# Kernel tuning notes

Hardware: AMD Instinct MI355X
Metric: run time of the kernel (lower is better)

Reference implementation:

```python
import jax, jax.numpy as jnp
import numpy as np

K_TOP = 4
NUM_EXPERTS = 8


def _lstm_dir(x, wih, whh, b):
    # x: [B,T,in], wih: [4H,in], whh: [4H,H], b: [4H] (b_ih+b_hh)
    xW = jnp.einsum('bti,gi->btg', x, wih) + b  # [B,T,4H]
    B = x.shape[0]
    H = whh.shape[1]
    init = (jnp.zeros((B, H), x.dtype), jnp.zeros((B, H), x.dtype))

    def step(carry, xt):
        h, c = carry
        g = xt + h @ whh.T
        i, f, gg, o = jnp.split(g, 4, axis=-1)  # torch gate order i,f,g,o
        c = jax.nn.sigmoid(f) * c + jax.nn.sigmoid(i) * jnp.tanh(gg)
        h = jax.nn.sigmoid(o) * jnp.tanh(c)
        return (h, c), h

    _, hs = jax.lax.scan(step, init, jnp.swapaxes(xW, 0, 1))  # [T,B,H]
    return jnp.swapaxes(hs, 0, 1)


def _bidir_layer(x, Wih, Whh, bih, bhh):
    # Wih: [2,4H,in]; dir 0 forward, dir 1 backward
    hf = _lstm_dir(x, Wih[0], Whh[0], bih[0] + bhh[0])
    hb = _lstm_dir(x[:, ::-1], Wih[1], Whh[1], bih[1] + bhh[1])[:, ::-1]
    return jnp.concatenate([hf, hb], axis=-1)  # [B,T,2H]


def _expert(x, Wih0, Whh0, bih0, bhh0, Wih1, Whh1, bih1, bhh1):
    h = _bidir_layer(x, Wih0, Whh0, bih0, bhh0)   # [B,T,2H]
    h = _bidir_layer(h, Wih1, Whh1, bih1, bhh1)   # [B,T,2H]
    return h


def _cv_squared(v):
    v = v.astype(jnp.float32)
    return jnp.var(v, ddof=1) / (jnp.mean(v) ** 2 + 1e-10)


def _forward(x, spk, wg_w, wg_b, Wih0, Whh0, bih0, bhh0, Wih1, Whh1, bih1, bhh1, fc1_w, fc1_b, fc_w, fc_b, loss_coef=0.01):
    B, T, _ = x.shape
    # --- top-k gating (eval path: clean logits, no noise) ---
    logits = spk @ wg_w.T + wg_b                      # [B,E]
    top_vals, top_idx = jax.lax.top_k(logits, K_TOP + 1)
    gates_k = jax.nn.softmax(top_vals[:, :K_TOP], axis=-1)
    rows = jnp.arange(B)[:, None]
    gates = jnp.zeros_like(logits).at[rows, top_idx[:, :K_TOP]].set(gates_k)  # [B,E]
    load = (gates > 0).sum(0)
    importance = gates.sum(0)
    loss = (_cv_squared(importance) + _cv_squared(load)) * loss_coef
    # --- run all experts (dense mixture, as in source) ---
    expert_h = jax.vmap(_expert, in_axes=(None, 0, 0, 0, 0, 0, 0, 0, 0))(
        x, Wih0, Whh0, bih0, bhh0, Wih1, Whh1, bih1, bhh1)          # [E,B,T,2H]
    expert_out = jnp.einsum('ebtf,hf->ebth', expert_h, fc1_w) + fc1_b  # [E,B,T,H]
    data_output = jnp.einsum('ebth,be->bth', expert_out, gates)        # [B,T,H]
    out = jnp.einsum('bth,oh->bto', data_output, fc_w) + fc_b          # [B,T,O]
    out = jnp.swapaxes(out, 0, 1)                                      # [T,B,O]
    return out, loss


def setup_inputs() -> dict:
    key = jax.random.key(0)
    ks = jax.random.split(key, 16)
    B, T, D, H, E, O, S = 32, 1024, 128, 128, 8, 44, 256
    s = 0.08  # weight scale to keep LSTM gates in sane range
    return {
        'x': jax.random.normal(ks[0], (B, T, D), jnp.float32),
        'spk': jax.random.normal(ks[1], (B, S), jnp.float32),
        'wg_w': jax.random.normal(ks[2], (E, S), jnp.float32) * s,
        'wg_b': jax.random.normal(ks[3], (E,), jnp.float32) * s,
        'Wih0': jax.random.normal(ks[4], (E, 2, 4 * H, D), jnp.float32) * s,
        'Whh0': jax.random.normal(ks[5], (E, 2, 4 * H, H), jnp.float32) * s,
        'bih0': jax.random.normal(ks[6], (E, 2, 4 * H), jnp.float32) * s,
        'bhh0': jax.random.normal(ks[7], (E, 2, 4 * H), jnp.float32) * s,
        'Wih1': jax.random.normal(ks[8], (E, 2, 4 * H, 2 * H), jnp.float32) * s,
        'Whh1': jax.random.normal(ks[9], (E, 2, 4 * H, H), jnp.float32) * s,
        'bih1': jax.random.normal(ks[10], (E, 2, 4 * H), jnp.float32) * s,
        'bhh1': jax.random.normal(ks[11], (E, 2, 4 * H), jnp.float32) * s,
        'fc1_w': jax.random.normal(ks[12], (H, 2 * H), jnp.float32) * s,
        'fc1_b': jax.random.normal(ks[13], (H,), jnp.float32) * s,
        'fc_w': jax.random.normal(ks[14], (O, H), jnp.float32) * s,
        'fc_b': jax.random.normal(ks[15], (O,), jnp.float32) * s,
    }


def reference(x, spk, wg_w, wg_b, Wih0, Whh0, bih0, bhh0, Wih1, Whh1, bih1, bhh1, fc1_w, fc1_b, fc_w, fc_b):
    return _forward(x, spk, wg_w, wg_b, Wih0, Whh0, bih0, bhh0, Wih1, Whh1, bih1, bhh1, fc1_w, fc1_b, fc_w, fc_b)
```

## Files before the change

### kernel.cpp

```cpp
#include <hip/hip_runtime.h>

typedef __attribute__((ext_vector_type(4))) float f32x4;
typedef __attribute__((ext_vector_type(8))) short s16x8;

#define LOG2E 1.4426950408889634f

__device__ __forceinline__ unsigned short f2bf(float f) {
  union { float f; unsigned int i; } v; v.f = f;
  unsigned int u = v.i;
  u = (u + 0x7FFFu + ((u >> 16) & 1u)) >> 16;
  return (unsigned short)u;
}
__device__ __forceinline__ float bf2f(unsigned short s) {
  union { unsigned int i; float f; } v; v.i = ((unsigned int)s) << 16;
  return v.f;
}
__device__ __forceinline__ float rcp_(float x) { return __builtin_amdgcn_rcpf(x); }
__device__ __forceinline__ float ex2(float x) { return __builtin_amdgcn_exp2f(x); }
__device__ __forceinline__ f32x4 mfma16(s16x8 a, s16x8 b, f32x4 c) {
  return __builtin_amdgcn_mfma_f32_16x16x32_bf16(a, b, c, 0, 0, 0);
}
__device__ __forceinline__ s16x8 pack8(const float* s) {
  s16x8 v;
#pragma unroll
  for (int j = 0; j < 8; ++j) v[j] = (short)f2bf(s[j]);
  return v;
}

#define OFF_H0  0
#define OFF_XW  134217728
#define OFF_XT  201326592
#define OFF_WHH 209715200
#define OFF_HST 213909504
#define OFF_CST 214040576
#define OFF_M   214564864
#define OFF_CV  214614016
#define OFF_G   214614272
#define WS_NEED 214615296

__global__ void wsdbg_kernel(float* __restrict__ out, float v) { out[0] = v; }

__global__ void prepw_kernel(const float* __restrict__ Whh0, const float* __restrict__ Whh1,
                             unsigned short* __restrict__ whhb) {
  const int i = blockIdx.x * 512 + threadIdx.x;
  if (i < 2097152)
    whhb[i] = f2bf(i < 1048576 ? Whh0[i] : Whh1[i - 1048576]);
}

__global__ void prepx_kernel(const float* __restrict__ x, unsigned short* __restrict__ xt) {
  const int i = blockIdx.x * 512 + threadIdx.x;
  for (int j = i; j < 4194304; j += 2097152) {
    const int b = j >> 17, rem = j & 131071, t = rem >> 7, f = rem & 127;
    xt[((size_t)t * 32 + b) * 128 + f] = f2bf(x[j]);
  }
}

__global__ void mprep_kernel(const float* __restrict__ fc1w, const float* __restrict__ fc1b,
                             const float* __restrict__ fcw, const float* __restrict__ fcb,
                             float* __restrict__ M, float* __restrict__ Cv) {
  const int mi = blockIdx.x * 256 + threadIdx.x;
  if (mi < 12288) {
    const int dd = mi / 6144, rem = mi % 6144, o = rem >> 7, hc = rem & 127;
    float s = 0.f;
    if (o < 44)
      for (int h = 0; h < 128; ++h) s += fcw[o * 128 + h] * fc1w[h * 256 + dd * 128 + hc];
    M[mi] = s;
  }
  if (blockIdx.x == 0 && threadIdx.x < 44) {
    const int o = threadIdx.x;
    float s = fcb[o];
    for (int h = 0; h < 128; ++h) s += fcw[o * 128 + h] * fc1b[h];
    Cv[o] = s;
  }
}

__global__ void initout_kernel(const float* __restrict__ Cv, float* __restrict__ out) {
  const int i = blockIdx.x * 512 + threadIdx.x;
  if (i < 1441792) out[i] = Cv[i % 44];
}

__global__ void gating_kernel(const float* __restrict__ spk,
                              const float* __restrict__ wgw,
                              const float* __restrict__ wgb,
                              float* __restrict__ gates_out,
                              float* __restrict__ loss_out) {
  __shared__ __align__(16) float logits[32][8];
  __shared__ __align__(16) float gmat[32][8];
  const int tid = threadIdx.x;
  {
    const int b = tid >> 3, e = tid & 7;
    float s = wgb[e];
    for (int k = 0; k < 256; ++k) s += spk[b * 256 + k] * wgw[e * 256 + k];
    logits[b][e] = s;
  }
  __syncthreads();
  if (tid < 32) {
    const int b = tid;
    float v[8];
    for (int e = 0; e < 8; ++e) v[e] = logits[b][e];
    int idx[4]; float val[4];
    unsigned used = 0;
    for (int k = 0; k < 4; ++k) {
      float best = -1e30f; int bi = 0;
      for (int e = 0; e < 8; ++e)
        if (!((used >> e) & 1) && v[e] > best) { best = v[e]; bi = e; }
      used |= (1u << bi); idx[k] = bi; val[k] = best;
    }
    const float m = val[0];
    float ex[4], ssum = 0.f;
    for (int k = 0; k < 4; ++k) { ex[k] = ex2(LOG2E * (val[k] - m)); ssum += ex[k]; }
    for (int e = 0; e < 8; ++e) gmat[b][e] = 0.f;
    for (int k = 0; k < 4; ++k) gmat[b][idx[k]] = ex[k] / ssum;
    for (int e = 0; e < 8; ++e) gates_out[b * 8 + e] = gmat[b][e];
  }
  __syncthreads();
  if (tid == 0) {
    float imp[8], ld[8];
    for (int e = 0; e < 8; ++e) {
      float si = 0.f, sl = 0.f;
      for (int b = 0; b < 32; ++b) { si += gmat[b][e]; sl += (gmat[b][e] > 0.f) ? 1.f : 0.f; }
      imp[e] = si; ld[e] = sl;
    }
    float mi = 0.f, ml = 0.f;
    for (int e = 0; e < 8; ++e) { mi += imp[e]; ml += ld[e]; }
    mi *= 0.125f; ml *= 0.125f;
    float vi = 0.f, vl = 0.f;
    for (int e = 0; e < 8; ++e) {
      vi += (imp[e] - mi) * (imp[e] - mi);
      vl += (ld[e] - ml) * (ld[e] - ml);
    }
    vi /= 7.f; vl /= 7.f;
    loss_out[0] = 0.01f * (vi / (mi * mi + 1e-10f) + vl / (ml * ml + 1e-10f));
  }
}

template <int L>
__global__ __launch_bounds__(512, 1) void fused(
    int k,
    const unsigned short* __restrict__ Asrc,
    const float* __restrict__ Wih, const float* __restrict__ bihp, const float* __restrict__ bhhp,
    const unsigned short* __restrict__ whhb,
    unsigned short* __restrict__ xwbufs,
    unsigned short* __restrict__ hstate, float* __restrict__ cstate,
    unsigned short* __restrict__ h0out,
    const float* __restrict__ Mmat, const float* __restrict__ gatesp,
    float* __restrict__ outp) {
  constexpr int KC = L ? 8 : 4;
  constexpr int KS = KC * 32;
  const int tid = threadIdx.x, w = tid >> 6, l = tid & 63;
  const int l15 = l & 15, lq = l >> 4;

  if (blockIdx.x >= 32) {
    if (k >= 16) return;
    const int gb = blockIdx.x - 32;
    const int ed = gb & 15, e = ed >> 1, d = ed & 1;
    const int slice = gb >> 4;
    unsigned short* xw = xwbufs + (size_t)(k & 1) * 16777216;

    s16x8 bf[4][KC];
    float bias[4];
#pragma unroll
    for (int j = 0; j < 4; ++j) {
      const int n = w * 64 + j * 16 + l15;
      bias[j] = bihp[ed * 512 + n] + bhhp[ed * 512 + n];
      const float* wp = Wih + ((size_t)ed * 512 + n) * KS + lq * 8;
#pragma unroll
      for (int kc = 0; kc < KC; ++kc) bf[j][kc] = pack8(wp + kc * 32);
    }
    for (int ss = slice; ss < 64; ss += 14) {
      const int s = k * 64 + ss;
      const int t = d ? 1023 - s : s;
#pragma unroll
      for (int mt = 0; mt < 2; ++mt) {
        const size_t arow = (size_t)(L ? (e * 1024 + t) : t) * 32 + mt * 16 + l15;
        const unsigned short* ap = Asrc + arow * KS + lq * 8;
        s16x8 af[KC];
#pragma unroll
        for (int kc = 0; kc < KC; ++kc) af[kc] = *(const s16x8*)(ap + kc * 32);
        f32x4 acc[4];
#pragma unroll
        for (int j = 0; j < 4; ++j) acc[j] = f32x4{bias[j], bias[j], bias[j], bias[j]};
#pragma unroll
        for (int kc = 0; kc < KC; ++kc) {
#pragma unroll
          for (int j = 0; j < 4; ++j) acc[j] = mfma16(af[kc], bf[j][kc], acc[j]);
        }
        unsigned short* op = xw + (((size_t)(ed * 2 + mt) * 64 + ss) * 512) * 16 + lq * 4;
#pragma unroll
        for (int j = 0; j < 4; ++j) {
          const int n = w * 64 + j * 16 + l15;
          ushort4 o4;
          o4.x = f2bf(acc[j][0]); o4.y = f2bf(acc[j][1]);
          o4.z = f2bf(acc[j][2]); o4.w = f2bf(acc[j][3]);
          *(ushort4*)(op + (size_t)n * 16) = o4;
        }
      }
    }
    return;
  }

  if (k == 0) return;
  const int c = k - 1;
  const int rb = blockIdx.x, ed2 = rb >> 1, bh = rb & 1;
  const int e = ed2 >> 1, d = ed2 & 1;
  __shared__ __align__(16) char hbf[2][4096];
  const int cell = w * 16 + l15;

  s16x8 bfh[4][4];
#pragma unroll
  for (int g = 0; g < 4; ++g) {
    const unsigned short* wp = whhb + ((size_t)ed2 * 512 + g * 128 + cell) * 128 + lq * 8;
#pragma unroll
    for (int kc = 0; kc < 4; ++kc) bfh[g][kc] = *(const s16x8*)(wp + kc * 32);
  }
  s16x8 mfr[4];
  float g4[4] = {0.f, 0.f, 0.f, 0.f};
  if constexpr (L) {
    if (w < 3) {
      const float* mp = Mmat + ((size_t)d * 48 + w * 16 + l15) * 128 + lq * 8;
#pragma unroll
      for (int kc = 0; kc < 4; ++kc) mfr[kc] = pack8(mp + kc * 32);
    }
#pragma unroll
    for (int r = 0; r < 4; ++r) g4[r] = gatesp[(bh * 16 + lq * 4 + r) * 8 + e];
  }

  const int wbase = ((cell >> 5) << 10) | (((cell >> 3) & 3) << 8) | ((cell & 7) << 1);
  float cst[4];
  if (c == 0) {
#pragma unroll
    for (int r = 0; r < 4; ++r) cst[r] = 0.f;
    if (tid < 256) {
      s16x8 z = {0, 0, 0, 0, 0, 0, 0, 0};
      *(s16x8*)(&hbf[0][tid * 16]) = z;
    }
  } else {
    const float* cp = cstate + ((size_t)rb * 512 + tid) * 4;
    const unsigned short* hp = hstate + ((size_t)rb * 512 + tid) * 4;
#pragma unroll
    for (int r = 0; r < 4; ++r) {
      cst[r] = cp[r];
      *(unsigned short*)(&hbf[0][wbase + (lq * 4 + r) * 16]) = hp[r];
    }
  }
  __syncthreads();

  const unsigned short* xwr = xwbufs + (size_t)(c & 1) * 16777216;
  const unsigned short* xwb = xwr + ((size_t)(ed2 * 2 + bh) * 64) * 8192 + cell * 16 + lq * 4;
  const size_t hob = (size_t)e * 8388608 + (size_t)(bh * 16 + lq * 4) * 256 + (size_t)d * 128 + cell;

  ushort4 xqA[4], xqB[4];
#pragma unroll
  for (int g = 0; g < 4; ++g) {
    xqA[g] = *(const ushort4*)(xwb + g * 2048);
    xqB[g] = *(const ushort4*)(xwb + 8192 + g * 2048);
  }

  auto step = [&](int tt, ushort4* xq, int tpre) {
    const int p = tt & 1;
    s16x8 hf[4];
#pragma unroll
    for (int kc = 0; kc < 4; ++kc) hf[kc] = *(const s16x8*)(&hbf[p][kc * 1024 + l * 16]);
    f32x4 a[4];
#pragma unroll
    for (int g = 0; g < 4; ++g) {
      a[g][0] = bf2f(xq[g].x); a[g][1] = bf2f(xq[g].y);
      a[g][2] = bf2f(xq[g].z); a[g][3] = bf2f(xq[g].w);
    }
    if (tpre < 64) {
#pragma unroll
      for (int g = 0; g < 4; ++g) xq[g] = *(const ushort4*)(xwb + (size_t)tpre * 8192 + g * 2048);
    }
    f32x4 mo = {0.f, 0.f, 0.f, 0.f};
    if constexpr (L) {
      if (w < 3) {
#pragma unroll
        for (int kc = 0; kc < 4; ++kc) mo = mfma16(hf[kc], mfr[kc], mo);
      }
    }
#pragma unroll
    for (int kc = 0; kc < 4; ++kc) {
#pragma unroll
      for (int g = 0; g < 4; ++g) a[g] = mfma16(hf[kc], bfh[g][kc], a[g]);
    }
    const int s = c * 64 + tt;
    unsigned short hb4[4];
#pragma unroll
    for (int r = 0; r < 4; ++r) {
      const float gi = a[0][r], gf = a[1][r], gg = a[2][r], go = a[3][r];
      const float ai = ex2(-LOG2E * gi);
      const float af2 = ex2(-LOG2E * gf);
      const float ao = ex2(-LOG2E * go);
      const float bg = ex2(fminf(2.f * LOG2E * gg, 126.f));
      const float sf = rcp_(1.f + af2);
      const float itg = (bg - 1.f) * rcp_((1.f + ai) * (1.f + bg));
      const float cc = sf * cst[r] + itg;
      cst[r] = cc;
      const float qc = ex2(fminf(2.f * LOG2E * cc, 126.f));
      const float hv = (qc - 1.f) * rcp_((1.f + ao) * (1.f + qc));
      hb4[r] = f2bf(hv);
    }
    char* hw = &hbf[1 - p][0];
#pragma unroll
    for (int r = 0; r < 4; ++r) *(unsigned short*)(hw + wbase + (lq * 4 + r) * 16) = hb4[r];
    if constexpr (!L) {
      const int t = d ? 1023 - s : s;
      unsigned short* hp = h0out + hob + (size_t)t * 8192;
#pragma unroll
      for (int r = 0; r < 4; ++r) hp[r * 256] = hb4[r];
    } else {
      if (w < 3 && s > 0) {
        const int o = w * 16 + l15;
        if (o < 44) {
          const int tp = d ? (1024 - s) : (s - 1);
#pragma unroll
          for (int r = 0; r < 4; ++r)
            atomicAdd(&outp[((size_t)tp * 32 + bh * 16 + lq * 4 + r) * 44 + o], g4[r] * mo[r]);
        }
      }
    }
    if (tt == 63) {
      unsigned short* hsp = hstate + ((size_t)rb * 512 + tid) * 4;
      float* csp = cstate + ((size_t)rb * 512 + tid) * 4;
#pragma unroll
      for (int r = 0; r < 4; ++r) { hsp[r] = hb4[r]; csp[r] = cst[r]; }
    }
    __syncthreads();
  };

  for (int t2 = 0; t2 < 64; t2 += 2) {
    step(t2, xqA, t2 + 2);
    step(t2 + 1, xqB, t2 + 3);
  }

  if constexpr (L) {
    if (k == 16 && w < 3) {
      s16x8 hf[4];
#pragma unroll
      for (int kc = 0; kc < 4; ++kc) hf[kc] = *(const s16x8*)(&hbf[0][kc * 1024 + l * 16]);
      f32x4 mo = {0.f, 0.f, 0.f, 0.f};
#pragma unroll
      for (int kc = 0; kc < 4; ++kc) mo = mfma16(hf[kc], mfr[kc], mo);
      const int o = w * 16 + l15;
      if (o < 44) {
        const int tp = d ? 0 : 1023;
#pragma unroll
        for (int r = 0; r < 4; ++r)
          atomicAdd(&outp[((size_t)tp * 32 + bh * 16 + lq * 4 + r) * 44 + o], g4[r] * mo[r]);
      }
    }
  }
}

extern "C" void kernel_launch(void* const* d_in, const int* in_sizes, int n_in,
                              void* d_out, int out_size, void* d_ws, size_t ws_size,
                              hipStream_t stream) {
  const float* x    = (const float*)d_in[0];
  const float* spk  = (const float*)d_in[1];
  const float* wgw  = (const float*)d_in[2];
  const float* wgb  = (const float*)d_in[3];
  const float* Wih0 = (const float*)d_in[4];
  const float* Whh0 = (const float*)d_in[5];
  const float* bih0 = (const float*)d_in[6];
  const float* bhh0 = (const float*)d_in[7];
  const float* Wih1 = (const float*)d_in[8];
  const float* Whh1 = (const float*)d_in[9];
  const float* bih1 = (const float*)d_in[10];
  const float* bhh1 = (const float*)d_in[11];
  const float* fc1w = (const float*)d_in[12];
  const float* fc1b = (const float*)d_in[13];
  const float* fcw  = (const float*)d_in[14];
  const float* fcb  = (const float*)d_in[15];
  float* out = (float*)d_out;

  if (ws_size < (size_t)WS_NEED) {
    wsdbg_kernel<<<1, 1, 0, stream>>>(out, (float)(ws_size >> 20));
    return;
  }
  char* ws = (char*)d_ws;
  unsigned short* h0     = (unsigned short*)(ws + OFF_H0);
  unsigned short* xwbufs = (unsigned short*)(ws + OFF_XW);
  unsigned short* xt     = (unsigned short*)(ws + OFF_XT);
  unsigned short* whhb   = (unsigned short*)(ws + OFF_WHH);
  unsigned short* hstate = (unsigned short*)(ws + OFF_HST);
  float*          cstate = (float*)(ws + OFF_CST);
  float*          Mmat   = (float*)(ws + OFF_M);
  float*          Cv     = (float*)(ws + OFF_CV);
  float*          gatesw = (float*)(ws + OFF_G);

  prepw_kernel<<<4096, 512, 0, stream>>>(Whh0, Whh1, whhb);
  prepx_kernel<<<4096, 512, 0, stream>>>(x, xt);
  mprep_kernel<<<48, 256, 0, stream>>>(fc1w, fc1b, fcw, fcb, Mmat, Cv);
  initout_kernel<<<2816, 512, 0, stream>>>(Cv, out);
  gating_kernel<<<1, 256, 0, stream>>>(spk, wgw, wgb, gatesw, out + 1441792);

  for (int k = 0; k <= 16; ++k)
    fused<0><<<256, 512, 0, stream>>>(k, xt, Wih0, bih0, bhh0, whhb, xwbufs,
                                      hstate, cstate, h0, nullptr, nullptr, out);
  for (int k = 0; k <= 16; ++k)
    fused<1><<<256, 512, 0, stream>>>(k, h0, Wih1, bih1, bhh1, whhb + 1048576, xwbufs,
                                      hstate, cstate, nullptr, Mmat, gatesw, out);
}
```

Measured before the change: 2.409 ms.

## Move layer-1 output projection to dedicated blocks and prescale gate weights

Gate weights and biases are now pre-multiplied by the exp2 scale factors, so the recurrent step's activation math needs fewer multiplies. The per-step output projection and atomicAdd in layer 1 are moved out of the recurrent blocks into separate blocks (192+). Those blocks process a double-buffered chunk of saved hidden states one launch later, reduce over experts with gate weights, and write output with plain adds. The recurrent step is rewritten as a single loop with the hidden-state store deferred by one step, and an extra launch is added to drain the pipeline. This trades more workspace and reduced input-projection parallelism in layer 1 for a shorter serial critical path.

```diff
diff --git a/kernel.cpp b/kernel.cpp
--- a/kernel.cpp
+++ b/kernel.cpp
@@ -4,6 +4,7 @@
 typedef __attribute__((ext_vector_type(8))) short s16x8;
 
 #define LOG2E 1.4426950408889634f
+#define K2L   2.8853900817779268f
 
 __device__ __forceinline__ unsigned short f2bf(float f) {
   union { float f; unsigned int i; } v; v.f = f;
@@ -20,31 +21,35 @@
 __device__ __forceinline__ f32x4 mfma16(s16x8 a, s16x8 b, f32x4 c) {
   return __builtin_amdgcn_mfma_f32_16x16x32_bf16(a, b, c, 0, 0, 0);
 }
-__device__ __forceinline__ s16x8 pack8(const float* s) {
+__device__ __forceinline__ s16x8 pack8s(const float* s, float sc) {
   s16x8 v;
 #pragma unroll
-  for (int j = 0; j < 8; ++j) v[j] = (short)f2bf(s[j]);
+  for (int j = 0; j < 8; ++j) v[j] = (short)f2bf(s[j] * sc);
   return v;
 }
 
-#define OFF_H0  0
-#define OFF_XW  134217728
-#define OFF_XT  201326592
-#define OFF_WHH 209715200
-#define OFF_HST 213909504
-#define OFF_CST 214040576
-#define OFF_M   214564864
-#define OFF_CV  214614016
-#define OFF_G   214614272
-#define WS_NEED 214615296
+#define OFF_H0   0
+#define OFF_XW   134217728
+#define OFF_XT   201326592
+#define OFF_WHH  209715200
+#define OFF_H1C  213909504
+#define OFF_HST  230686720
+#define OFF_CST  230817792
+#define OFF_M    231079936
+#define OFF_CV   231129088
+#define OFF_G    231129344
+#define WS_NEED  231130368
 
 __global__ void wsdbg_kernel(float* __restrict__ out, float v) { out[0] = v; }
 
 __global__ void prepw_kernel(const float* __restrict__ Whh0, const float* __restrict__ Whh1,
                              unsigned short* __restrict__ whhb) {
   const int i = blockIdx.x * 512 + threadIdx.x;
-  if (i < 2097152)
-    whhb[i] = f2bf(i < 1048576 ? Whh0[i] : Whh1[i - 1048576]);
+  if (i < 2097152) {
+    const int gate = (i >> 14) & 3;
+    const float sc = (gate == 2) ? K2L : -LOG2E;
+    whhb[i] = f2bf((i < 1048576 ? Whh0[i] : Whh1[i - 1048576]) * sc);
+  }
 }
 
 __global__ void prepx_kernel(const float* __restrict__ x, unsigned short* __restrict__ xt) {
@@ -142,7 +147,7 @@
     const unsigned short* __restrict__ whhb,
     unsigned short* __restrict__ xwbufs,
     unsigned short* __restrict__ hstate, float* __restrict__ cstate,
-    unsigned short* __restrict__ h0out,
+    unsigned short* __restrict__ hout,
     const float* __restrict__ Mmat, const float* __restrict__ gatesp,
     float* __restrict__ outp) {
   constexpr int KC = L ? 8 : 4;
@@ -150,11 +155,59 @@
   const int tid = threadIdx.x, w = tid >> 6, l = tid & 63;
   const int l15 = l & 15, lq = l >> 4;
 
+  if (L && blockIdx.x >= 192) {
+    const int c2 = k - 2;
+    if (c2 < 0 || c2 > 15) return;
+    if (w >= 6) return;
+    const int ss = blockIdx.x - 192;
+    const int mt = (w >= 3) ? 1 : 0, ot = w - mt * 3;
+    const int o = ot * 16 + l15;
+    const bool ov = o < 44;
+    s16x8 bfm[2][4];
+#pragma unroll
+    for (int dd = 0; dd < 2; ++dd)
+#pragma unroll
+      for (int kc = 0; kc < 4; ++kc) {
+        if (ov) bfm[dd][kc] = pack8s(Mmat + ((size_t)dd * 48 + o) * 128 + kc * 32 + lq * 8, 1.f);
+        else { s16x8 z = {0,0,0,0,0,0,0,0}; bfm[dd][kc] = z; }
+      }
+    const unsigned short* hb = hout + (size_t)(c2 & 1) * 4194304;
+    f32x4 acc0 = {0.f,0.f,0.f,0.f}, acc1 = {0.f,0.f,0.f,0.f};
+    for (int e = 0; e < 8; ++e) {
+      const unsigned short* ap = hb + ((((size_t)e * 64 + ss) * 32) + mt * 16 + l15) * 256 + lq * 8;
+      f32x4 p0 = {0.f,0.f,0.f,0.f}, p1 = {0.f,0.f,0.f,0.f};
+#pragma unroll
+      for (int kc = 0; kc < 4; ++kc) {
+        s16x8 a0 = *(const s16x8*)(ap + kc * 32);
+        s16x8 a1 = *(const s16x8*)(ap + 128 + kc * 32);
+        p0 = mfma16(a0, bfm[0][kc], p0);
+        p1 = mfma16(a1, bfm[1][kc], p1);
+      }
+#pragma unroll
+      for (int r = 0; r < 4; ++r) {
+        const float g = gatesp[(mt * 16 + lq * 4 + r) * 8 + e];
+        acc0[r] += g * p0[r];
+        acc1[r] += g * p1[r];
+      }
+    }
+    if (ov) {
+      const int s2 = c2 * 64 + ss, t1 = 1023 - s2;
+#pragma unroll
+      for (int r = 0; r < 4; ++r) {
+        const int b = mt * 16 + lq * 4 + r;
+        outp[((size_t)s2 * 32 + b) * 44 + o] += acc0[r];
+        outp[((size_t)t1 * 32 + b) * 44 + o] += acc1[r];
+      }
+    }
+    return;
+  }
+
   if (blockIdx.x >= 32) {
     if (k >= 16) return;
     const int gb = blockIdx.x - 32;
     const int ed = gb & 15, e = ed >> 1, d = ed & 1;
     const int slice = gb >> 4;
+    const int nsl = L ? 10 : 14;
     unsigned short* xw = xwbufs + (size_t)(k & 1) * 16777216;
 
     s16x8 bf[4][KC];
@@ -162,12 +215,13 @@
 #pragma unroll
     for (int j = 0; j < 4; ++j) {
       const int n = w * 64 + j * 16 + l15;
-      bias[j] = bihp[ed * 512 + n] + bhhp[ed * 512 + n];
+      const float sc = ((n >> 7) == 2) ? K2L : -LOG2E;
+      bias[j] = (bihp[ed * 512 + n] + bhhp[ed * 512 + n]) * sc;
       const float* wp = Wih + ((size_t)ed * 512 + n) * KS + lq * 8;
 #pragma unroll
-      for (int kc = 0; kc < KC; ++kc) bf[j][kc] = pack8(wp + kc * 32);
-    }
-    for (int ss = slice; ss < 64; ss += 14) {
+      for (int kc = 0; kc < KC; ++kc) bf[j][kc] = pack8s(wp + kc * 32, sc);
+    }
+    for (int ss = slice; ss < 64; ss += nsl) {
       const int s = k * 64 + ss;
       const int t = d ? 1023 - s : s;
 #pragma unroll
@@ -199,8 +253,8 @@
     return;
   }
 
-  if (k == 0) return;
   const int c = k - 1;
+  if (c < 0 || c > 15) return;
   const int rb = blockIdx.x, ed2 = rb >> 1, bh = rb & 1;
   const int e = ed2 >> 1, d = ed2 & 1;
   __shared__ __align__(16) char hbf[2][4096];
@@ -213,25 +267,14 @@
 #pragma unroll
     for (int kc = 0; kc < 4; ++kc) bfh[g][kc] = *(const s16x8*)(wp + kc * 32);
   }
-  s16x8 mfr[4];
-  float g4[4] = {0.f, 0.f, 0.f, 0.f};
-  if constexpr (L) {
-    if (w < 3) {
-      const float* mp = Mmat + ((size_t)d * 48 + w * 16 + l15) * 128 + lq * 8;
-#pragma unroll
-      for (int kc = 0; kc < 4; ++kc) mfr[kc] = pack8(mp + kc * 32);
-    }
-#pragma unroll
-    for (int r = 0; r < 4; ++r) g4[r] = gatesp[(bh * 16 + lq * 4 + r) * 8 + e];
-  }
-
-  const int wbase = ((cell >> 5) << 10) | (((cell >> 3) & 3) << 8) | ((cell & 7) << 1);
+  const int wb0 = ((cell >> 5) << 10) | (((cell >> 3) & 3) << 8) | ((cell & 7) << 1);
   float cst[4];
+  unsigned short hb4[4];
   if (c == 0) {
 #pragma unroll
-    for (int r = 0; r < 4; ++r) cst[r] = 0.f;
+    for (int r = 0; r < 4; ++r) { cst[r] = 0.f; hb4[r] = 0; }
     if (tid < 256) {
-      s16x8 z = {0, 0, 0, 0, 0, 0, 0, 0};
+      s16x8 z = {0,0,0,0,0,0,0,0};
       *(s16x8*)(&hbf[0][tid * 16]) = z;
     }
   } else {
@@ -240,24 +283,42 @@
 #pragma unroll
     for (int r = 0; r < 4; ++r) {
       cst[r] = cp[r];
-      *(unsigned short*)(&hbf[0][wbase + (lq * 4 + r) * 16]) = hp[r];
+      hb4[r] = hp[r];
+      *(unsigned short*)(&hbf[0][wb0 | ((lq * 4 + r) << 4)]) = hp[r];
     }
   }
   __syncthreads();
 
-  const unsigned short* xwr = xwbufs + (size_t)(c & 1) * 16777216;
-  const unsigned short* xwb = xwr + ((size_t)(ed2 * 2 + bh) * 64) * 8192 + cell * 16 + lq * 4;
-  const size_t hob = (size_t)e * 8388608 + (size_t)(bh * 16 + lq * 4) * 256 + (size_t)d * 128 + cell;
-
-  ushort4 xqA[4], xqB[4];
-#pragma unroll
-  for (int g = 0; g < 4; ++g) {
-    xqA[g] = *(const ushort4*)(xwb + g * 2048);
-    xqB[g] = *(const ushort4*)(xwb + 8192 + g * 2048);
-  }
-
-  auto step = [&](int tt, ushort4* xq, int tpre) {
+  const unsigned short* xwb =
+      xwbufs + (size_t)(c & 1) * 16777216 + ((size_t)(ed2 * 2 + bh) * 64) * 8192 + cell * 16 + lq * 4;
+  const int brow = bh * 16 + lq * 4;
+
+  ushort4 xq[4];
+#pragma unroll
+  for (int g = 0; g < 4; ++g) xq[g] = *(const ushort4*)(xwb + g * 2048);
+
+  for (int tt = 0; tt < 64; ++tt) {
     const int p = tt & 1;
+    ushort4 nxq[4];
+    {
+      const int tn = tt < 63 ? tt + 1 : 63;
+#pragma unroll
+      for (int g = 0; g < 4; ++g) nxq[g] = *(const ushort4*)(xwb + (size_t)tn * 8192 + g * 2048);
+    }
+    if (tt > 0) {
+      const int ptt = tt - 1;
+      size_t ob;
+      if (L) {
+        ob = (size_t)(c & 1) * 4194304 + (((size_t)e * 64 + ptt) * 32 + brow) * 256 + d * 128 + cell;
+      } else {
+        const int s = c * 64 + ptt;
+        const int tg = d ? 1023 - s : s;
+        ob = (((size_t)e * 1024 + tg) * 32 + brow) * 256 + d * 128 + cell;
+      }
+#pragma unroll
+      for (int r = 0; r < 4; ++r) hout[ob + (size_t)r * 256] = hb4[r];
+    }
+
     s16x8 hf[4];
 #pragma unroll
     for (int kc = 0; kc < 4; ++kc) hf[kc] = *(const s16x8*)(&hbf[p][kc * 1024 + l * 16]);
@@ -267,88 +328,51 @@
       a[g][0] = bf2f(xq[g].x); a[g][1] = bf2f(xq[g].y);
       a[g][2] = bf2f(xq[g].z); a[g][3] = bf2f(xq[g].w);
     }
-    if (tpre < 64) {
-#pragma unroll
-      for (int g = 0; g < 4; ++g) xq[g] = *(const ushort4*)(xwb + (size_t)tpre * 8192 + g * 2048);
-    }
-    f32x4 mo = {0.f, 0.f, 0.f, 0.f};
-    if constexpr (L) {
-      if (w < 3) {
-#pragma unroll
-        for (int kc = 0; kc < 4; ++kc) mo = mfma16(hf[kc], mfr[kc], mo);
-      }
-    }
 #pragma unroll
     for (int kc = 0; kc < 4; ++kc) {
 #pragma unroll
       for (int g = 0; g < 4; ++g) a[g] = mfma16(hf[kc], bfh[g][kc], a[g]);
     }
-    const int s = c * 64 + tt;
-    unsigned short hb4[4];
+
 #pragma unroll
     for (int r = 0; r < 4; ++r) {
-      const float gi = a[0][r], gf = a[1][r], gg = a[2][r], go = a[3][r];
-      const float ai = ex2(-LOG2E * gi);
-      const float af2 = ex2(-LOG2E * gf);
-      const float ao = ex2(-LOG2E * go);
-      const float bg = ex2(fminf(2.f * LOG2E * gg, 126.f));
-      const float sf = rcp_(1.f + af2);
-      const float itg = (bg - 1.f) * rcp_((1.f + ai) * (1.f + bg));
-      const float cc = sf * cst[r] + itg;
+      const float ai = ex2(a[0][r]);
+      const float af = ex2(a[1][r]);
+      const float bg = ex2(fminf(a[2][r], 80.f));
+      const float ao = ex2(a[3][r]);
+      const float sf = rcp_(1.f + af);
+      const float r1 = rcp_((1.f + ai) * (1.f + bg));
+      const float bgm = __builtin_fmaf(bg, K2L, -K2L);
+      const float cc = __builtin_fmaf(sf, cst[r], bgm * r1);
       cst[r] = cc;
-      const float qc = ex2(fminf(2.f * LOG2E * cc, 126.f));
-      const float hv = (qc - 1.f) * rcp_((1.f + ao) * (1.f + qc));
-      hb4[r] = f2bf(hv);
+      const float qc = ex2(fminf(cc, 80.f));
+      const float r2 = rcp_((1.f + ao) * (1.f + qc));
+      hb4[r] = f2bf((qc - 1.f) * r2);
     }
     char* hw = &hbf[1 - p][0];
 #pragma unroll
-    for (int r = 0; r < 4; ++r) *(unsigned short*)(hw + wbase + (lq * 4 + r) * 16) = hb4[r];
-    if constexpr (!L) {
-      const int t = d ? 1023 - s : s;
-      unsigned short* hp = h0out + hob + (size_t)t * 8192;
-#pragma unroll
-      for (int r = 0; r < 4; ++r) hp[r * 256] = hb4[r];
+    for (int r = 0; r < 4; ++r)
+      *(unsigned short*)(hw + (wb0 | ((lq * 4 + r) << 4))) = hb4[r];
+    __syncthreads();
+#pragma unroll
+    for (int g = 0; g < 4; ++g) xq[g] = nxq[g];
+  }
+
+  {
+    size_t ob;
+    if (L) {
+      ob = (size_t)(c & 1) * 4194304 + (((size_t)e * 64 + 63) * 32 + brow) * 256 + d * 128 + cell;
     } else {
-      if (w < 3 && s > 0) {
-        const int o = w * 16 + l15;
-        if (o < 44) {
-          const int tp = d ? (1024 - s) : (s - 1);
-#pragma unroll
-          for (int r = 0; r < 4; ++r)
-            atomicAdd(&outp[((size_t)tp * 32 + bh * 16 + lq * 4 + r) * 44 + o], g4[r] * mo[r]);
-        }
-      }
-    }
-    if (tt == 63) {
-      unsigned short* hsp = hstate + ((size_t)rb * 512 + tid) * 4;
-      float* csp = cstate + ((size_t)rb * 512 + tid) * 4;
-#pragma unroll
-      for (int r = 0; r < 4; ++r) { hsp[r] = hb4[r]; csp[r] = cst[r]; }
-    }
-    __syncthreads();
-  };
-
-  for (int t2 = 0; t2 < 64; t2 += 2) {
-    step(t2, xqA, t2 + 2);
-    step(t2 + 1, xqB, t2 + 3);
-  }
-
-  if constexpr (L) {
-    if (k == 16 && w < 3) {
-      s16x8 hf[4];
-#pragma unroll
-      for (int kc = 0; kc < 4; ++kc) hf[kc] = *(const s16x8*)(&hbf[0][kc * 1024 + l * 16]);
-      f32x4 mo = {0.f, 0.f, 0.f, 0.f};
-#pragma unroll
-      for (int kc = 0; kc < 4; ++kc) mo = mfma16(hf[kc], mfr[kc], mo);
-      const int o = w * 16 + l15;
-      if (o < 44) {
-        const int tp = d ? 0 : 1023;
-#pragma unroll
-        for (int r = 0; r < 4; ++r)
-          atomicAdd(&outp[((size_t)tp * 32 + bh * 16 + lq * 4 + r) * 44 + o], g4[r] * mo[r]);
-      }
-    }
+      const int s = c * 64 + 63;
+      const int tg = d ? 1023 - s : s;
+      ob = (((size_t)e * 1024 + tg) * 32 + brow) * 256 + d * 128 + cell;
+    }
+#pragma unroll
+    for (int r = 0; r < 4; ++r) hout[ob + (size_t)r * 256] = hb4[r];
+    unsigned short* hsp = hstate + ((size_t)rb * 512 + tid) * 4;
+    float* csp = cstate + ((size_t)rb * 512 + tid) * 4;
+#pragma unroll
+    for (int r = 0; r < 4; ++r) { hsp[r] = hb4[r]; csp[r] = cst[r]; }
   }
 }
 
@@ -382,6 +406,7 @@
   unsigned short* xwbufs = (unsigned short*)(ws + OFF_XW);
   unsigned short* xt     = (unsigned short*)(ws + OFF_XT);
   unsigned short* whhb   = (unsigned short*)(ws + OFF_WHH);
+  unsigned short* h1c    = (unsigned short*)(ws + OFF_H1C);
   unsigned short* hstate = (unsigned short*)(ws + OFF_HST);
   float*          cstate = (float*)(ws + OFF_CST);
   float*          Mmat   = (float*)(ws + OFF_M);
@@ -397,7 +422,7 @@
   for (int k = 0; k <= 16; ++k)
     fused<0><<<256, 512, 0, stream>>>(k, xt, Wih0, bih0, bhh0, whhb, xwbufs,
                                       hstate, cstate, h0, nullptr, nullptr, out);
-  for (int k = 0; k <= 16; ++k)
+  for (int k = 0; k <= 17; ++k)
     fused<1><<<256, 512, 0, stream>>>(k, h0, Wih1, bih1, bhh1, whhb + 1048576, xwbufs,
-                                      hstate, cstate, nullptr, Mmat, gatesw, out);
-}
+                                      hstate, cstate, h1c, Mmat, gatesw, out);
+}
```

After: 2.076 ms. 13.8% less time.
